# Optimization experiments

Hardware: AMD Instinct MI355X
Metric: run time of the kernel (lower is better)

Reference implementation:

```python
import jax, jax.numpy as jnp
import numpy as np

B, C, H, W = 4, 64, 64, 64
CQ = C // 2

def setup_inputs() -> dict:
    key = jax.random.key(0)
    ks = jax.random.split(key, 7)
    return {
        "x":  jax.random.normal(ks[0], (B, C, H, W), dtype=jnp.float32),
        "Wq": jax.random.normal(ks[1], (CQ, C), dtype=jnp.float32) * 0.05,
        "bq": jax.random.normal(ks[2], (CQ,), dtype=jnp.float32) * 0.05,
        "Wk": jax.random.normal(ks[3], (CQ, C), dtype=jnp.float32) * 0.05,
        "bk": jax.random.normal(ks[4], (CQ,), dtype=jnp.float32) * 0.05,
        "Wl": jax.random.normal(ks[5], (C, C), dtype=jnp.float32) * 0.05,
        "bl": jax.random.normal(ks[6], (C,), dtype=jnp.float32) * 0.05,
    }

def reference(x, Wq, bq, Wk, bk, Wl, bl):
    b, c, h, w = x.shape
    hw = h * w
    xf = x.reshape(b, c, hw)                                   # [B,C,HW]
    # 1x1 convs == per-pixel linear projections
    q = jnp.einsum('oc,bci->boi', Wq, xf) + bq[None, :, None]  # [B,CQ,HW]
    k = jnp.einsum('oc,bci->boi', Wk, xf) + bk[None, :, None]  # [B,CQ,HW]
    # energy[b,i,j] = <q[:,i], k[:,j]>  (proj_query permuted to [B,HW,CQ])
    energy = jnp.einsum('bci,bcj->bij', q, k)                  # [B,HW,HW]
    attn = jax.nn.softmax(energy, axis=-1)                     # softmax over last dim (keys j)
    # torch.bmm(proj_value, attention): out[b,c,j] = sum_i value[b,c,i] * attn[b,i,j]
    out = jnp.einsum('bci,bij->bcj', xf, attn)                 # [B,C,HW]
    out = out.reshape(b, c, h, w)
    out = jnp.einsum('oc,bchw->bohw', Wl, out) + bl[None, :, None, None]
    return out + x
```

## Files before the change

### kernel.cpp

```cpp
#include <hip/hip_runtime.h>
#include <hip/hip_bf16.h>


#define HW 4096
#define BN 4
#define CD 64
#define ISPL 8
#define LOG2E 1.44269504f

typedef short bf16x8 __attribute__((ext_vector_type(8)));
typedef float f32x4 __attribute__((ext_vector_type(4)));

static __device__ inline unsigned bfbits(float f) {
    union { float f; unsigned u; } v{f};
    return (v.u + 0x8000u) >> 16;
}
static __device__ inline float b2f(short s) {
    unsigned u = ((unsigned)(unsigned short)s) << 16;
    float f; __builtin_memcpy(&f, &u, 4); return f;
}
static __device__ inline int cvtpk(float lo, float hi) {
    __hip_bfloat162 h = __float22bfloat162_rn(make_float2(lo, hi));
    int r; __builtin_memcpy(&r, &h, 4); return r;
}
static __device__ inline void gl16(const void* g, void* l) {
    __builtin_amdgcn_global_load_lds(
        (const __attribute__((address_space(1))) unsigned int*)g,
        (__attribute__((address_space(3))) unsigned int*)l, 16, 0, 0);
}



__global__ __launch_bounds__(256, 4) void k_proj(
    const float* __restrict__ x, const float* __restrict__ Wq, const float* __restrict__ bq,
    const float* __restrict__ Wk, const float* __restrict__ bk, const float* __restrict__ Wl,
    short* __restrict__ Qt, short* __restrict__ Kt, short* __restrict__ Yc)
{
    __shared__ __align__(16) char sm[18944];
    short* WcL   = (short*)sm;
    short* xT    = (short*)(sm + 16384);
    float* biasL = (float*)(sm + 18432);

    int t = threadIdx.x;
    int wv = t >> 6, l = t & 63, g = l >> 4, n = l & 15;

    {
        int row = t >> 1, half = t & 1;
        const float* src; float scale = 1.f;
        if (row < 32)      { src = Wq + row * CD; scale = LOG2E; }
        else if (row < 64) { src = Wk + (row - 32) * CD; }
        else               { src = Wl + (row - 64) * CD; }
        int pk[16];
#pragma unroll
        for (int e = 0; e < 16; ++e)
            pk[e] = cvtpk(src[half * 32 + 2 * e] * scale, src[half * 32 + 2 * e + 1] * scale);
#pragma unroll
        for (int q = 0; q < 4; ++q)
            *(int4*)(WcL + row * 64 + ((((half << 2) + q) ^ (row & 7)) << 3)) =
                make_int4(pk[4 * q], pk[4 * q + 1], pk[4 * q + 2], pk[4 * q + 3]);
        if (half == 0)
            biasL[row] = (row < 32) ? LOG2E * bq[row] : (row < 64) ? bk[row - 32] : 0.f;
    }
    int pix0 = blockIdx.x << 4;
    {
        int c = t >> 2, q = t & 3;
        int b = pix0 >> 12, pxb = pix0 & (HW - 1);
        float4 v = *(const float4*)(x + ((size_t)b << 18) + ((size_t)c << 12) + pxb + q * 4);
        float vv[4] = {v.x, v.y, v.z, v.w};
#pragma unroll
        for (int e = 0; e < 4; ++e) {
            int px = q * 4 + e;
            xT[px * 64 + (((c >> 3) ^ (px & 7)) << 3) + (c & 7)] = (short)bfbits(vv[e]);
        }
    }
    __syncthreads();

    bf16x8 B0 = *(const bf16x8*)(xT + n * 64 + ((g ^ (n & 7)) << 3));
    bf16x8 B1 = *(const bf16x8*)(xT + n * 64 + (((4 + g) ^ (n & 7)) << 3));
    int pg = pix0 + n;
#pragma unroll
    for (int mm = 0; mm < 2; ++mm) {
        int mt = wv * 2 + mm;
        bf16x8 A0 = *(const bf16x8*)(WcL + (mt * 16 + n) * 64 + ((g ^ (n & 7)) << 3));
        bf16x8 A1 = *(const bf16x8*)(WcL + (mt * 16 + n) * 64 + (((4 + g) ^ (n & 7)) << 3));
        f32x4 d = {0.f, 0.f, 0.f, 0.f};
        d = __builtin_amdgcn_mfma_f32_16x16x32_bf16(A0, B0, d, 0, 0, 0);
        d = __builtin_amdgcn_mfma_f32_16x16x32_bf16(A1, B1, d, 0, 0, 0);
        d += *(const f32x4*)(biasL + mt * 16 + g * 4);
        if (mt < 4) {
            short* dst = (mt < 2 ? Qt : Kt) + ((size_t)pg << 5) + ((mt & 1) << 4) + (g << 2);
            *(int2*)dst = make_int2(cvtpk(d[0], d[1]), cvtpk(d[2], d[3]));
        } else {
            int ch2 = (mt - 4) * 16 + g * 4;
            int bb = pg >> 12, ii = pg & (HW - 1);
#pragma unroll
            for (int r = 0; r < 4; ++r)
                Yc[(((size_t)(bb * CD + ch2 + r)) << 12) + ii] = (short)bfbits(d[r]);
        }
    }
}


__global__ __launch_bounds__(256, 4) void k_pass1m(
    const short* __restrict__ Qt, const short* __restrict__ Kt, float* __restrict__ Spart)
{
    __shared__ float red[256];
    int t = threadIdx.x;
    int wv = t >> 6, l = t & 63, g = l >> 4, n = l & 15;
    int ch = blockIdx.x;
    int b = ch & 3, jq = (ch >> 2) & 3, i0 = (ch >> 4) << 6;
    size_t bHW = (size_t)b << 12;

    bf16x8 aq[4];
#pragma unroll
    for (int it = 0; it < 4; ++it)
        aq[it] = *(const bf16x8*)(Qt + ((bHW + i0 + it * 16 + n) << 5) + (g << 3));

    f32x4 ls[4];
#pragma unroll
    for (int it = 0; it < 4; ++it) ls[it] = (f32x4){0.f, 0.f, 0.f, 0.f};

    const short* kbase = Kt + ((bHW + jq * 1024 + wv * 256 + n) << 5) + (g << 3);
#pragma unroll 4
    for (int jt = 0; jt < 16; ++jt) {
        bf16x8 bkv = *(const bf16x8*)(kbase + jt * 512);
#pragma unroll
        for (int it = 0; it < 4; ++it) {
            f32x4 z = {0.f, 0.f, 0.f, 0.f};
            f32x4 s = __builtin_amdgcn_mfma_f32_16x16x32_bf16(aq[it], bkv, z, 0, 0, 0);
            ls[it][0] += exp2f(s[0]); ls[it][1] += exp2f(s[1]);
            ls[it][2] += exp2f(s[2]); ls[it][3] += exp2f(s[3]);
        }
    }
#pragma unroll
    for (int msk = 1; msk < 16; msk <<= 1)
#pragma unroll
        for (int it = 0; it < 4; ++it) {
            ls[it][0] += __shfl_xor(ls[it][0], msk, 64);
            ls[it][1] += __shfl_xor(ls[it][1], msk, 64);
            ls[it][2] += __shfl_xor(ls[it][2], msk, 64);
            ls[it][3] += __shfl_xor(ls[it][3], msk, 64);
        }
    if (n == 0)
#pragma unroll
        for (int it = 0; it < 4; ++it)
#pragma unroll
            for (int r = 0; r < 4; ++r)
                red[wv * 64 + it * 16 + g * 4 + r] = ls[it][r];
    __syncthreads();
    if (t < 64) {
        float s = red[t] + red[64 + t] + red[128 + t] + red[192 + t];
        Spart[(size_t)jq * 16384 + bHW + i0 + t] = s;
    }
}


__global__ __launch_bounds__(256, 4) void k_pass2(
    const short* __restrict__ Qt, const short* __restrict__ Kt,
    const short* __restrict__ Yc, const float* __restrict__ Spart,
    short* __restrict__ Opart)
{
    __shared__ __align__(16) char smem[36864];
    short* QtL = (short*)smem;
    short* W2L = (short*)(smem + 8192);
    short* Pb  = (short*)(smem + 24576);
    float* MtA = (float*)(smem + 34816);

    int t = threadIdx.x;
    int wv = t >> 6, l = t & 63, g = l >> 4, n = l & 15;
    int ch = blockIdx.x;
    int b = ch >> 8, isp = (ch >> 5) & 7, jt = ch & 31;
    int j0 = jt * 128 + wv * 32;
    size_t bHW = (size_t)b << 12;
    short* Pw = Pb + wv * 1280;

    bf16x8 bk0 = *(const bf16x8*)(Kt + ((bHW + j0 + n) << 5) + (g << 3));
    bf16x8 bk1 = *(const bf16x8*)(Kt + ((bHW + j0 + 16 + n) << 5) + (g << 3));

    f32x4 oacc[2][4];
#pragma unroll
    for (int a = 0; a < 2; ++a)
#pragma unroll
        for (int m = 0; m < 4; ++m) oacc[a][m] = (f32x4){0.f, 0.f, 0.f, 0.f};

    int swz = ((t & 7) ^ ((t >> 3) & 7)) << 4;
    const char* qsrc = (const char*)Qt + ((bHW + (size_t)isp * 512) << 6) + t * 16;
    const char* wsrc = (const char*)Yc + (((size_t)(b * CD + (t >> 3)) << 12) + isp * 512) * 2 + swz;
    char* qd0 = (char*)QtL + t * 16;  char* qd1 = qd0 + 4096;
    char* wd0 = (char*)W2L + t * 16;  char* wd1 = wd0 + 8192;

    gl16(qsrc, qd0);
    gl16(wsrc, wd0);
    gl16(wsrc + (32ull << 13), wd0 + 4096);
    if (t < 128) {
        const float* sp = Spart + bHW + (size_t)isp * 512 + t * 4;
        float4 a0 = *(const float4*)(sp);
        float4 a1 = *(const float4*)(sp + 16384);
        float4 a2 = *(const float4*)(sp + 32768);
        float4 a3 = *(const float4*)(sp + 49152);
        float4 mm;
        mm.x = -log2f(a0.x + a1.x + a2.x + a3.x);
        mm.y = -log2f(a0.y + a1.y + a2.y + a3.y);
        mm.z = -log2f(a0.z + a1.z + a2.z + a3.z);
        mm.w = -log2f(a0.w + a1.w + a2.w + a3.w);
        *(float4*)(MtA + t * 4) = mm;
    }
    asm volatile("s_waitcnt vmcnt(0) lgkmcnt(0)" ::: "memory");
    __builtin_amdgcn_s_barrier();
    __builtin_amdgcn_sched_barrier(0);

    const int NT = 8;
    for (int st = 0; st < NT; ++st) {
        int cur = st & 1;
        if (st > 0) {
            __builtin_amdgcn_s_barrier();
            __builtin_amdgcn_sched_barrier(0);
        }
        if (st + 1 < NT) {
            gl16(qsrc + (size_t)(st + 1) * 4096, cur ? qd0 : qd1);
            gl16(wsrc + (size_t)(st + 1) * 128, cur ? wd0 : wd1);
            gl16(wsrc + (size_t)(st + 1) * 128 + (32ull << 13), (cur ? wd0 : wd1) + 4096);
            asm volatile("s_waitcnt vmcnt(3)" ::: "memory");
        } else {
            asm volatile("s_waitcnt vmcnt(0)" ::: "memory");
        }
        __builtin_amdgcn_sched_barrier(0);

        const short* qL = QtL + cur * 2048;
        const char* wL = (const char*)W2L + cur * 8192;
        const float* mL = MtA + st * 64;
#pragma unroll
        for (int ks = 0; ks < 2; ++ks) {
            bf16x8 aq0 = *(const bf16x8*)(qL + (ks * 32 + n) * 32 + g * 8);
            bf16x8 aq1 = *(const bf16x8*)(qL + (ks * 32 + 16 + n) * 32 + g * 8);
            f32x4 cm0 = *(const f32x4*)(mL + ks * 32 + g * 4);
            f32x4 cm1 = *(const f32x4*)(mL + ks * 32 + 16 + g * 4);
            __builtin_amdgcn_s_setprio(1);
            f32x4 s00 = __builtin_amdgcn_mfma_f32_16x16x32_bf16(aq0, bk0, cm0, 0, 0, 0);
            f32x4 s01 = __builtin_amdgcn_mfma_f32_16x16x32_bf16(aq1, bk0, cm1, 0, 0, 0);
            f32x4 s10 = __builtin_amdgcn_mfma_f32_16x16x32_bf16(aq0, bk1, cm0, 0, 0, 0);
            f32x4 s11 = __builtin_amdgcn_mfma_f32_16x16x32_bf16(aq1, bk1, cm1, 0, 0, 0);
            __builtin_amdgcn_s_setprio(0);
            *(int2*)(Pw + n * 40 + 4 * g) =
                make_int2(cvtpk(exp2f(s00[0]), exp2f(s00[1])), cvtpk(exp2f(s00[2]), exp2f(s00[3])));
            *(int2*)(Pw + n * 40 + 16 + 4 * g) =
                make_int2(cvtpk(exp2f(s01[0]), exp2f(s01[1])), cvtpk(exp2f(s01[2]), exp2f(s01[3])));
            *(int2*)(Pw + (16 + n) * 40 + 4 * g) =
                make_int2(cvtpk(exp2f(s10[0]), exp2f(s10[1])), cvtpk(exp2f(s10[2]), exp2f(s10[3])));
            *(int2*)(Pw + (16 + n) * 40 + 16 + 4 * g) =
                make_int2(cvtpk(exp2f(s11[0]), exp2f(s11[1])), cvtpk(exp2f(s11[2]), exp2f(s11[3])));
            bf16x8 pb0 = *(const bf16x8*)(Pw + n * 40 + 8 * g);
            bf16x8 pb1 = *(const bf16x8*)(Pw + (16 + n) * 40 + 8 * g);
            __builtin_amdgcn_s_setprio(1);
#pragma unroll
            for (int mb = 0; mb < 4; ++mb) {
                bf16x8 aw = *(const bf16x8*)(wL + (mb * 16 + n) * 128 + ((((ks << 2) + g) ^ (n & 7)) << 4));
                oacc[0][mb] = __builtin_amdgcn_mfma_f32_16x16x32_bf16(aw, pb0, oacc[0][mb], 0, 0, 0);
                oacc[1][mb] = __builtin_amdgcn_mfma_f32_16x16x32_bf16(aw, pb1, oacc[1][mb], 0, 0, 0);
            }
            __builtin_amdgcn_s_setprio(0);
        }
        __builtin_amdgcn_sched_barrier(0);
    }
    size_t obase = ((((size_t)isp * BN + b) * CD) << 12) + j0 + n;
#pragma unroll
    for (int j2 = 0; j2 < 2; ++j2)
#pragma unroll
        for (int mb = 0; mb < 4; ++mb)
#pragma unroll
            for (int r = 0; r < 4; ++r)
                Opart[obase + (((size_t)(mb * 16 + g * 4 + r)) << 12) + j2 * 16] =
                    (short)bfbits(oacc[j2][mb][r]);
}


__global__ __launch_bounds__(256, 4) void k_merge(
    const short* __restrict__ Opart, const float* __restrict__ x,
    const float* __restrict__ bl, float* __restrict__ out)
{
    int t = threadIdx.x;
    int e = (blockIdx.x * 256 + t) * 4;
    int c = (e >> 12) & 63;
    float4 r = *(const float4*)(x + e);
    float bc = bl[c];
    r.x += bc; r.y += bc; r.z += bc; r.w += bc;
#pragma unroll
    for (int p = 0; p < ISPL; ++p) {
        int2 o4 = *(const int2*)(Opart + ((size_t)p << 20) + e);
        r.x += b2f((short)(o4.x & 0xffff));
        r.y += b2f((short)(o4.x >> 16));
        r.z += b2f((short)(o4.y & 0xffff));
        r.w += b2f((short)(o4.y >> 16));
    }
    *(float4*)(out + e) = r;
}

extern "C" void kernel_launch(void* const* d_in, const int* in_sizes, int n_in,
                              void* d_out, int out_size, void* d_ws, size_t ws_size,
                              hipStream_t stream)
{
    (void)in_sizes; (void)n_in; (void)out_size; (void)ws_size;
    const float* x  = (const float*)d_in[0];
    const float* Wq = (const float*)d_in[1];
    const float* bq = (const float*)d_in[2];
    const float* Wk = (const float*)d_in[3];
    const float* bk = (const float*)d_in[4];
    const float* Wl = (const float*)d_in[5];
    const float* bl = (const float*)d_in[6];
    float* out = (float*)d_out;
    char* base = (char*)d_ws;

    short* Qt    = (short*)(base);
    short* Kt    = (short*)(base + 0x100000);
    short* Yc    = (short*)(base + 0x200000);
    float* Spart = (float*)(base + 0x500000);
    short* Opart = (short*)(base + 0x540000);

    hipLaunchKernelGGL(k_proj, dim3(1024), dim3(256), 0, stream,
                       x, Wq, bq, Wk, bk, Wl, Qt, Kt, Yc);
    hipLaunchKernelGGL(k_pass1m, dim3(1024), dim3(256), 0, stream, Qt, Kt, Spart);
    hipLaunchKernelGGL(k_pass2, dim3(1024), dim3(256), 0, stream,
                       Qt, Kt, Yc, Spart, Opart);
    hipLaunchKernelGGL(k_merge, dim3(1024), dim3(256), 0, stream, Opart, x, bl, out);
}
```

Measured before the change: 62.31 us.

## Restructure attention pass2 into 512-thread blocks with fewer key-split partials

The attention-value pass now runs 512-thread blocks of 8 waves, each wave owning 16 output columns. Each block covers 1024 query rows over 16 stages, so the key split drops from 8 to 4. Shared Q and value tiles are staged once per block and reused by twice as many waves, and the partial-output buffer plus the merge kernel's reads are halved. In exchange, each wave does half the MFMA work per stage, the serial loop is twice as long, and a larger block may limit occupancy and barrier overlap.

```diff
diff --git a/kernel.cpp b/kernel.cpp
--- a/kernel.cpp
+++ b/kernel.cpp
@@ -5,7 +5,7 @@
 #define HW 4096
 #define BN 4
 #define CD 64
-#define ISPL 8
+#define ISPL 4
 #define LOG2E 1.44269504f
 
 typedef short bf16x8 __attribute__((ext_vector_type(8)));
@@ -155,12 +155,12 @@
 }
 
 
-__global__ __launch_bounds__(256, 4) void k_pass2(
+__global__ __launch_bounds__(512, 4) void k_pass2(
     const short* __restrict__ Qt, const short* __restrict__ Kt,
     const short* __restrict__ Yc, const float* __restrict__ Spart,
     short* __restrict__ Opart)
 {
-    __shared__ __align__(16) char smem[36864];
+    __shared__ __align__(16) char smem[38912];
     short* QtL = (short*)smem;
     short* W2L = (short*)(smem + 8192);
     short* Pb  = (short*)(smem + 24576);
@@ -169,31 +169,29 @@
     int t = threadIdx.x;
     int wv = t >> 6, l = t & 63, g = l >> 4, n = l & 15;
     int ch = blockIdx.x;
-    int b = ch >> 8, isp = (ch >> 5) & 7, jt = ch & 31;
-    int j0 = jt * 128 + wv * 32;
+    int b = ch >> 7, isp = (ch >> 5) & 3, jt = ch & 31;
+    int j0 = jt * 128 + wv * 16;
     size_t bHW = (size_t)b << 12;
-    short* Pw = Pb + wv * 1280;
+    short* Pw = Pb + wv * 640;
 
     bf16x8 bk0 = *(const bf16x8*)(Kt + ((bHW + j0 + n) << 5) + (g << 3));
-    bf16x8 bk1 = *(const bf16x8*)(Kt + ((bHW + j0 + 16 + n) << 5) + (g << 3));
-
-    f32x4 oacc[2][4];
-#pragma unroll
-    for (int a = 0; a < 2; ++a)
-#pragma unroll
-        for (int m = 0; m < 4; ++m) oacc[a][m] = (f32x4){0.f, 0.f, 0.f, 0.f};
+
+    f32x4 oacc[4];
+#pragma unroll
+    for (int m = 0; m < 4; ++m) oacc[m] = (f32x4){0.f, 0.f, 0.f, 0.f};
 
     int swz = ((t & 7) ^ ((t >> 3) & 7)) << 4;
-    const char* qsrc = (const char*)Qt + ((bHW + (size_t)isp * 512) << 6) + t * 16;
-    const char* wsrc = (const char*)Yc + (((size_t)(b * CD + (t >> 3)) << 12) + isp * 512) * 2 + swz;
-    char* qd0 = (char*)QtL + t * 16;  char* qd1 = qd0 + 4096;
+    const char* qsrc = (const char*)Qt + ((bHW + (size_t)isp * 1024) << 6)
+                     + wv * 512 + (l & 31) * 16;
+    const char* wsrc = (const char*)Yc + (((size_t)(b * CD + (t >> 3)) << 12) + isp * 1024) * 2 + swz;
+    char* qd0 = (char*)QtL + wv * 512;
+    char* qd1 = qd0 + 4096;
     char* wd0 = (char*)W2L + t * 16;  char* wd1 = wd0 + 8192;
 
-    gl16(qsrc, qd0);
+    if (l < 32) gl16(qsrc, qd0);
     gl16(wsrc, wd0);
-    gl16(wsrc + (32ull << 13), wd0 + 4096);
-    if (t < 128) {
-        const float* sp = Spart + bHW + (size_t)isp * 512 + t * 4;
+    if (t < 256) {
+        const float* sp = Spart + bHW + (size_t)isp * 1024 + t * 4;
         float4 a0 = *(const float4*)(sp);
         float4 a1 = *(const float4*)(sp + 16384);
         float4 a2 = *(const float4*)(sp + 32768);
@@ -209,7 +207,7 @@
     __builtin_amdgcn_s_barrier();
     __builtin_amdgcn_sched_barrier(0);
 
-    const int NT = 8;
+    const int NT = 16;
     for (int st = 0; st < NT; ++st) {
         int cur = st & 1;
         if (st > 0) {
@@ -217,10 +215,9 @@
             __builtin_amdgcn_sched_barrier(0);
         }
         if (st + 1 < NT) {
-            gl16(qsrc + (size_t)(st + 1) * 4096, cur ? qd0 : qd1);
+            if (l < 32) gl16(qsrc + (size_t)(st + 1) * 4096, cur ? qd0 : qd1);
             gl16(wsrc + (size_t)(st + 1) * 128, cur ? wd0 : wd1);
-            gl16(wsrc + (size_t)(st + 1) * 128 + (32ull << 13), (cur ? wd0 : wd1) + 4096);
-            asm volatile("s_waitcnt vmcnt(3)" ::: "memory");
+            asm volatile("s_waitcnt vmcnt(2)" ::: "memory");
         } else {
             asm volatile("s_waitcnt vmcnt(0)" ::: "memory");
         }
@@ -238,25 +235,17 @@
             __builtin_amdgcn_s_setprio(1);
             f32x4 s00 = __builtin_amdgcn_mfma_f32_16x16x32_bf16(aq0, bk0, cm0, 0, 0, 0);
             f32x4 s01 = __builtin_amdgcn_mfma_f32_16x16x32_bf16(aq1, bk0, cm1, 0, 0, 0);
-            f32x4 s10 = __builtin_amdgcn_mfma_f32_16x16x32_bf16(aq0, bk1, cm0, 0, 0, 0);
-            f32x4 s11 = __builtin_amdgcn_mfma_f32_16x16x32_bf16(aq1, bk1, cm1, 0, 0, 0);
             __builtin_amdgcn_s_setprio(0);
             *(int2*)(Pw + n * 40 + 4 * g) =
                 make_int2(cvtpk(exp2f(s00[0]), exp2f(s00[1])), cvtpk(exp2f(s00[2]), exp2f(s00[3])));
             *(int2*)(Pw + n * 40 + 16 + 4 * g) =
                 make_int2(cvtpk(exp2f(s01[0]), exp2f(s01[1])), cvtpk(exp2f(s01[2]), exp2f(s01[3])));
-            *(int2*)(Pw + (16 + n) * 40 + 4 * g) =
-                make_int2(cvtpk(exp2f(s10[0]), exp2f(s10[1])), cvtpk(exp2f(s10[2]), exp2f(s10[3])));
-            *(int2*)(Pw + (16 + n) * 40 + 16 + 4 * g) =
-                make_int2(cvtpk(exp2f(s11[0]), exp2f(s11[1])), cvtpk(exp2f(s11[2]), exp2f(s11[3])));
             bf16x8 pb0 = *(const bf16x8*)(Pw + n * 40 + 8 * g);
-            bf16x8 pb1 = *(const bf16x8*)(Pw + (16 + n) * 40 + 8 * g);
             __builtin_amdgcn_s_setprio(1);
 #pragma unroll
             for (int mb = 0; mb < 4; ++mb) {
                 bf16x8 aw = *(const bf16x8*)(wL + (mb * 16 + n) * 128 + ((((ks << 2) + g) ^ (n & 7)) << 4));
-                oacc[0][mb] = __builtin_amdgcn_mfma_f32_16x16x32_bf16(aw, pb0, oacc[0][mb], 0, 0, 0);
-                oacc[1][mb] = __builtin_amdgcn_mfma_f32_16x16x32_bf16(aw, pb1, oacc[1][mb], 0, 0, 0);
+                oacc[mb] = __builtin_amdgcn_mfma_f32_16x16x32_bf16(aw, pb0, oacc[mb], 0, 0, 0);
             }
             __builtin_amdgcn_s_setprio(0);
         }
@@ -264,13 +253,11 @@
     }
     size_t obase = ((((size_t)isp * BN + b) * CD) << 12) + j0 + n;
 #pragma unroll
-    for (int j2 = 0; j2 < 2; ++j2)
-#pragma unroll
-        for (int mb = 0; mb < 4; ++mb)
-#pragma unroll
-            for (int r = 0; r < 4; ++r)
-                Opart[obase + (((size_t)(mb * 16 + g * 4 + r)) << 12) + j2 * 16] =
-                    (short)bfbits(oacc[j2][mb][r]);
+    for (int mb = 0; mb < 4; ++mb)
+#pragma unroll
+        for (int r = 0; r < 4; ++r)
+            Opart[obase + (((size_t)(mb * 16 + g * 4 + r)) << 12)] =
+                (short)bfbits(oacc[mb][r]);
 }
 
 
@@ -319,7 +306,7 @@
     hipLaunchKernelGGL(k_proj, dim3(1024), dim3(256), 0, stream,
                        x, Wq, bq, Wk, bk, Wl, Qt, Kt, Yc);
     hipLaunchKernelGGL(k_pass1m, dim3(1024), dim3(256), 0, stream, Qt, Kt, Spart);
-    hipLaunchKernelGGL(k_pass2, dim3(1024), dim3(256), 0, stream,
+    hipLaunchKernelGGL(k_pass2, dim3(512), dim3(512), 0, stream,
                        Qt, Kt, Yc, Spart, Opart);
     hipLaunchKernelGGL(k_merge, dim3(1024), dim3(256), 0, stream, Opart, x, bl, out);
 }
```

New measurement: 63.58 us. 1.02x slower.
